# Kernel tuning notes

Measured on AMD Instinct MI355X. Metric: run time of the kernel, lower is better.

## Reference

```python
import jax, jax.numpy as jnp
import numpy as np

E = 32          # embed_size; each node embedding is an [E, E] matrix
V = 50257       # vocab size
L = 2048        # number of leaves (complete binary tree)
N = 2 * L - 1   # total nodes, post-order-compatible layout (children before parent)
LBL = 128       # label_size


def setup_inputs() -> dict:
    key = jax.random.key(0)
    k1, k2, k3 = jax.random.split(key, 3)
    words = jax.random.randint(k1, (N,), 0, V, dtype=jnp.int32)
    # complete binary tree: nodes 0..L-1 are leaves; internal node i has
    # children 2*(i-L) and 2*(i-L)+1, which always have smaller indices.
    left = np.zeros(N, dtype=np.int32)
    right = np.zeros(N, dtype=np.int32)
    ii = np.arange(L, N)
    left[L:] = 2 * (ii - L)
    right[L:] = left[L:] + 1
    is_leaf = np.arange(N) < L
    # xavier-ish init scale for embedding ([V, E*E]) and projection
    emb = jax.random.normal(k2, (V, E * E), dtype=jnp.float32) * (1.0 / E)
    bias = jnp.zeros((E, E), dtype=jnp.float32)
    W_proj = jax.random.normal(k3, (LBL, E * E), dtype=jnp.float32) * 0.02
    b_proj = jnp.zeros((LBL,), dtype=jnp.float32)
    return {
        "words": words,
        "left": jnp.asarray(left),
        "right": jnp.asarray(right),
        "is_leaf": jnp.asarray(is_leaf),
        "emb": emb,
        "bias": bias,
        "W_proj": W_proj,
        "b_proj": b_proj,
        "label": 3,
    }


def reference(words, left, right, is_leaf, emb, bias, W_proj, b_proj, label):
    n = words.shape[0]
    e = bias.shape[0]
    states0 = jnp.zeros((n, e, e), dtype=emb.dtype)

    def step(states, x):
        i, w, li, ri, leaf = x
        Wn = emb[w].reshape(e, e)                    # node embedding matrix
        l = states[li]                               # [E, E] child state
        r = states[ri]
        comp = l @ (Wn @ r) + bias                   # RNTN composition
        val = jnp.where(leaf, jax.nn.relu(Wn), jax.nn.relu(comp))
        return states.at[i].set(val), None

    xs = (jnp.arange(n), words, left, right, is_leaf)
    states, _ = jax.lax.scan(step, states0, xs)

    root = states[-1].reshape(-1)                    # [E*E]
    logits = root @ W_proj.T + b_proj                # [LBL]
    loss = -jax.nn.log_softmax(logits)[label]        # CrossEntropyLoss, batch=1
    prediction = jnp.argmax(logits)
    return prediction, loss
```

## Files before the change

### kernel.cpp

```cpp
#include <hip/hip_runtime.h>
#include <math.h>


#define EE 1024
typedef float4 f4;

__device__ __forceinline__ f4 relu4(f4 v) {
    v.x = fmaxf(v.x, 0.f); v.y = fmaxf(v.y, 0.f);
    v.z = fmaxf(v.z, 0.f); v.w = fmaxf(v.w, 0.f);
    return v;
}
__device__ __forceinline__ f4 fma4s(float s, f4 b, f4 a) {
    a.x = fmaf(s, b.x, a.x); a.y = fmaf(s, b.y, a.y);
    a.z = fmaf(s, b.z, a.z); a.w = fmaf(s, b.w, a.w);
    return a;
}
__device__ __forceinline__ f4 addrelu4(f4 a, f4 b) {
    a.x = fmaxf(a.x + b.x, 0.f); a.y = fmaxf(a.y + b.y, 0.f);
    a.z = fmaxf(a.z + b.z, 0.f); a.w = fmaxf(a.w + b.w, 0.f);
    return a;
}
__device__ __forceinline__ void lds_fence() {
    asm volatile("s_waitcnt lgkmcnt(0)" ::: "memory");
    __builtin_amdgcn_sched_barrier(0);
}
__device__ __forceinline__ void load_row(f4 d[4], const float* __restrict__ src, int lane) {
    #pragma unroll
    for (int i = 0; i < 4; ++i) d[i] = ((const f4*)src)[lane + 64 * i];
}

__device__ __forceinline__ void node_wave(
    const f4 wv[4], bool reluKids,
    const float* __restrict__ Lsrc, const float* __restrict__ Rsrc,
    const float* __restrict__ bias, int lane,
    float* sA, float* sB, float* gdst)
{
    f4 rv[4], lv[4];
    load_row(rv, Rsrc, lane);
    load_row(lv, Lsrc, lane);
    if (reluKids) {
        #pragma unroll
        for (int i = 0; i < 4; ++i) { rv[i] = relu4(rv[i]); lv[i] = relu4(lv[i]); }
    }
    #pragma unroll
    for (int i = 0; i < 4; ++i) {
        ((f4*)sA)[lane + 64 * i] = wv[i];
        ((f4*)sB)[lane + 64 * i] = rv[i];
    }
    lds_fence();

    const int tr = lane >> 3, tc = lane & 7;
    const f4 z = {0.f, 0.f, 0.f, 0.f};
    f4 t0 = z, t1 = z, t2 = z, t3 = z;
    #pragma unroll
    for (int k = 0; k < 32; k += 4) {
        f4 a0 = *(const f4*)(sA + (4 * tr + 0) * 32 + k);
        f4 a1 = *(const f4*)(sA + (4 * tr + 1) * 32 + k);
        f4 a2 = *(const f4*)(sA + (4 * tr + 2) * 32 + k);
        f4 a3 = *(const f4*)(sA + (4 * tr + 3) * 32 + k);
        f4 b0 = *(const f4*)(sB + (k + 0) * 32 + 4 * tc);
        f4 b1 = *(const f4*)(sB + (k + 1) * 32 + 4 * tc);
        f4 b2 = *(const f4*)(sB + (k + 2) * 32 + 4 * tc);
        f4 b3 = *(const f4*)(sB + (k + 3) * 32 + 4 * tc);
        t0 = fma4s(a0.x, b0, fma4s(a0.y, b1, fma4s(a0.z, b2, fma4s(a0.w, b3, t0))));
        t1 = fma4s(a1.x, b0, fma4s(a1.y, b1, fma4s(a1.z, b2, fma4s(a1.w, b3, t1))));
        t2 = fma4s(a2.x, b0, fma4s(a2.y, b1, fma4s(a2.z, b2, fma4s(a2.w, b3, t2))));
        t3 = fma4s(a3.x, b0, fma4s(a3.y, b1, fma4s(a3.z, b2, fma4s(a3.w, b3, t3))));
    }
    __builtin_amdgcn_sched_barrier(0);
    *(f4*)(sA + (4 * tr + 0) * 32 + 4 * tc) = t0;
    *(f4*)(sA + (4 * tr + 1) * 32 + 4 * tc) = t1;
    *(f4*)(sA + (4 * tr + 2) * 32 + 4 * tc) = t2;
    *(f4*)(sA + (4 * tr + 3) * 32 + 4 * tc) = t3;
    #pragma unroll
    for (int i = 0; i < 4; ++i) ((f4*)sB)[lane + 64 * i] = lv[i];
    lds_fence();

    f4 s0 = z, s1 = z, s2 = z, s3 = z;
    #pragma unroll
    for (int k = 0; k < 32; k += 4) {
        f4 a0 = *(const f4*)(sB + (4 * tr + 0) * 32 + k);
        f4 a1 = *(const f4*)(sB + (4 * tr + 1) * 32 + k);
        f4 a2 = *(const f4*)(sB + (4 * tr + 2) * 32 + k);
        f4 a3 = *(const f4*)(sB + (4 * tr + 3) * 32 + k);
        f4 b0 = *(const f4*)(sA + (k + 0) * 32 + 4 * tc);
        f4 b1 = *(const f4*)(sA + (k + 1) * 32 + 4 * tc);
        f4 b2 = *(const f4*)(sA + (k + 2) * 32 + 4 * tc);
        f4 b3 = *(const f4*)(sA + (k + 3) * 32 + 4 * tc);
        s0 = fma4s(a0.x, b0, fma4s(a0.y, b1, fma4s(a0.z, b2, fma4s(a0.w, b3, s0))));
        s1 = fma4s(a1.x, b0, fma4s(a1.y, b1, fma4s(a1.z, b2, fma4s(a1.w, b3, s1))));
        s2 = fma4s(a2.x, b0, fma4s(a2.y, b1, fma4s(a2.z, b2, fma4s(a2.w, b3, s2))));
        s3 = fma4s(a3.x, b0, fma4s(a3.y, b1, fma4s(a3.z, b2, fma4s(a3.w, b3, s3))));
    }
    s0 = addrelu4(s0, *(const f4*)(bias + (4 * tr + 0) * 32 + 4 * tc));
    s1 = addrelu4(s1, *(const f4*)(bias + (4 * tr + 1) * 32 + 4 * tc));
    s2 = addrelu4(s2, *(const f4*)(bias + (4 * tr + 2) * 32 + 4 * tc));
    s3 = addrelu4(s3, *(const f4*)(bias + (4 * tr + 3) * 32 + 4 * tc));
    *(f4*)(sB + (4 * tr + 0) * 32 + 4 * tc) = s0;
    *(f4*)(sB + (4 * tr + 1) * 32 + 4 * tc) = s1;
    *(f4*)(sB + (4 * tr + 2) * 32 + 4 * tc) = s2;
    *(f4*)(sB + (4 * tr + 3) * 32 + 4 * tc) = s3;
    if (gdst) {
        *(f4*)(gdst + (4 * tr + 0) * 32 + 4 * tc) = s0;
        *(f4*)(gdst + (4 * tr + 1) * 32 + 4 * tc) = s1;
        *(f4*)(gdst + (4 * tr + 2) * 32 + 4 * tc) = s2;
        *(f4*)(gdst + (4 * tr + 3) * 32 + 4 * tc) = s3;
    }
}

template<bool LEAF>
__global__ __launch_bounds__(256) void subtree_kernel(
    const int* __restrict__ words, const float* __restrict__ emb,
    const float* __restrict__ bias, float* __restrict__ states,
    int rootBase, int nCompute, const float* __restrict__ warm, int warmN, int L)
{
    __shared__ float sBuf[8 * EE];
    const int bid = blockIdx.x;
    const int t = threadIdx.x, w = t >> 6, lane = t & 63;
    if (bid >= nCompute) {
        float acc = 0.f;
        for (int i = (bid - nCompute) * 256 + t; i < 128 * EE / 4; i += warmN * 256) {
            const f4 v = ((const f4*)warm)[i];
            acc += v.x + v.y + v.z + v.w;
        }
        asm volatile("" :: "v"(acc));
        return;
    }
    const int root = rootBase + bid;
    const int c1i = 2 * (root - L) + (w >> 1);
    const int nbi = 2 * (c1i - L) + (w & 1);
    f4 wv[4], wx[4], wr[4];
    load_row(wv, emb + (size_t)words[nbi] * EE, lane);
    if (w < 2) load_row(wx, emb + (size_t)words[2 * (root - L) + w] * EE, lane);
    if (w == 0) load_row(wr, emb + (size_t)words[root] * EE, lane);
    const int li = 2 * (nbi - L), ri = li + 1;
    const float *Lp, *Rp;
    if (LEAF) { Lp = emb + (size_t)words[li] * EE;        Rp = emb + (size_t)words[ri] * EE; }
    else      { Lp = states + (size_t)(li - L) * EE;      Rp = states + (size_t)(ri - L) * EE; }

    node_wave(wv, LEAF, Lp, Rp, bias, lane,
              sBuf + 2 * w * EE, sBuf + (2 * w + 1) * EE, nullptr);
    __syncthreads();
    if (w < 2)
        node_wave(wx, false, sBuf + (4 * w + 1) * EE, sBuf + (4 * w + 3) * EE,
                  bias, lane, sBuf + 4 * w * EE, sBuf + (4 * w + 2) * EE, nullptr);
    __syncthreads();
    if (w == 0)
        node_wave(wr, false, sBuf + 2 * EE, sBuf + 6 * EE, bias, lane,
                  sBuf + 0 * EE, sBuf + 4 * EE, states + (size_t)(root - L) * EE);
}

__global__ __launch_bounds__(1024) void tail_kernel(
    const int* __restrict__ words, const float* __restrict__ emb,
    const float* __restrict__ bias, float* __restrict__ states,
    const float* __restrict__ W_proj, const float* __restrict__ b_proj,
    const int* __restrict__ label, float* __restrict__ out, int L, int N)
{
    __shared__ float sBuf[6 * EE];
    __shared__ float sLog[128];
    const int t = threadIdx.x, w = t >> 6, lane = t & 63;
    const int rootN = N - 1;

    f4 wv[4], wr[4];
    if (w < 2) {
        const int n = rootN - 2 + w;
        load_row(wv, emb + (size_t)words[n] * EE, lane);
        if (w == 0) load_row(wr, emb + (size_t)words[rootN] * EE, lane);
        const int li = 2 * (n - L), ri = li + 1;
        node_wave(wv, false, states + (size_t)(li - L) * EE,
                  states + (size_t)(ri - L) * EE, bias, lane,
                  sBuf + 2 * w * EE, sBuf + (2 * w + 1) * EE, nullptr);
    } else {
        float acc = 0.f;
        for (int i = t - 128; i < 128 * EE / 4; i += 896) {
            const f4 v = ((const f4*)W_proj)[i];
            acc += v.x + v.y + v.z + v.w;
        }
        asm volatile("" :: "v"(acc));
    }
    __syncthreads();
    if (w == 0)
        node_wave(wr, false, sBuf + 1 * EE, sBuf + 3 * EE, bias, lane,
                  sBuf + 4 * EE, sBuf + 5 * EE, nullptr);
    __syncthreads();

    const float* root = sBuf + 5 * EE;
    {
        const int j = t >> 3, part = t & 7;
        const float* Wr = W_proj + (size_t)j * EE + part * 128;
        const float* rt = root + part * 128;
        float acc = 0.f;
        #pragma unroll
        for (int k = 0; k < 128; k += 4) {
            const f4 w4 = *(const f4*)(Wr + k);
            const f4 r4 = *(const f4*)(rt + k);
            acc = fmaf(w4.x, r4.x, acc);
            acc = fmaf(w4.y, r4.y, acc);
            acc = fmaf(w4.z, r4.z, acc);
            acc = fmaf(w4.w, r4.w, acc);
        }
        acc += __shfl_xor(acc, 1);
        acc += __shfl_xor(acc, 2);
        acc += __shfl_xor(acc, 4);
        if (part == 0) sLog[j] = acc + b_proj[j];
    }
    __syncthreads();

    if (t < 64) {
        const float v0 = sLog[t], v1 = sLog[t + 64];
        float m; int mi;
        if (v1 > v0) { m = v1; mi = t + 64; } else { m = v0; mi = t; }
        #pragma unroll
        for (int d = 1; d < 64; d <<= 1) {
            const float om = __shfl_xor(m, d);
            const int omi = __shfl_xor(mi, d);
            if (om > m || (om == m && omi < mi)) { m = om; mi = omi; }
        }
        float se = expf(v0 - m) + expf(v1 - m);
        #pragma unroll
        for (int d = 1; d < 64; d <<= 1) se += __shfl_xor(se, d);
        if (t == 0) {
            out[0] = (float)mi;
            out[1] = -(sLog[label[0]] - m - logf(se));
        }
    }
}

extern "C" void kernel_launch(void* const* d_in, const int* in_sizes, int n_in,
                              void* d_out, int out_size, void* d_ws, size_t ws_size,
                              hipStream_t stream) {
    (void)n_in; (void)out_size; (void)ws_size;
    const int*   words  = (const int*)  d_in[0];
    const float* emb    = (const float*)d_in[4];
    const float* bias   = (const float*)d_in[5];
    const float* W_proj = (const float*)d_in[6];
    const float* b_proj = (const float*)d_in[7];
    const int*   label  = (const int*)  d_in[8];
    float* out    = (float*)d_out;
    float* states = (float*)d_ws;

    const int N = in_sizes[0];
    const int L = (N + 1) / 2;

    const int lv3 = L + L / 2 + L / 4;
    const int lv6 = lv3 + L / 8 + L / 16 + L / 32;
    const int lv9 = lv6 + L / 64 + L / 128 + L / 256;

    subtree_kernel<true><<<256, 256, 0, stream>>>(
        words, emb, bias, states, lv3, 256, W_proj, 8, L);
    subtree_kernel<false><<<40, 256, 0, stream>>>(
        words, emb, bias, states, lv6, 32, W_proj, 8, L);
    subtree_kernel<false><<<12, 256, 0, stream>>>(
        words, emb, bias, states, lv9, 4, W_proj, 8, L);
    tail_kernel<<<1, 1024, 0, stream>>>(
        words, emb, bias, states, W_proj, b_proj, label, out, L, N);
}
```

Before: 65.81 us.

## Fuse tree-level kernels into one cooperative kernel with grid syncs

Replaces the four sequential launches (three subtree levels plus the tail) with a single cooperative kernel of L/8 blocks that separates levels with grid-wide syncs. Block 0 then performs the top levels, projection and softmax itself. This removes the per-launch overhead and the gaps between kernels, in exchange for grid barrier costs and the requirement that all 256 blocks be co-resident. If the cooperative launch fails, the code falls back to the old multi-kernel path.

```diff
diff --git a/kernel.cpp b/kernel.cpp
--- a/kernel.cpp
+++ b/kernel.cpp
@@ -1,5 +1,8 @@
 #include <hip/hip_runtime.h>
+#include <hip/hip_cooperative_groups.h>
 #include <math.h>
+
+namespace cg = cooperative_groups;
 
 
 #define EE 1024
@@ -109,24 +112,11 @@
 }
 
 template<bool LEAF>
-__global__ __launch_bounds__(256) void subtree_kernel(
+__device__ __forceinline__ void do_subtree(
     const int* __restrict__ words, const float* __restrict__ emb,
     const float* __restrict__ bias, float* __restrict__ states,
-    int rootBase, int nCompute, const float* __restrict__ warm, int warmN, int L)
-{
-    __shared__ float sBuf[8 * EE];
-    const int bid = blockIdx.x;
-    const int t = threadIdx.x, w = t >> 6, lane = t & 63;
-    if (bid >= nCompute) {
-        float acc = 0.f;
-        for (int i = (bid - nCompute) * 256 + t; i < 128 * EE / 4; i += warmN * 256) {
-            const f4 v = ((const f4*)warm)[i];
-            acc += v.x + v.y + v.z + v.w;
-        }
-        asm volatile("" :: "v"(acc));
-        return;
-    }
-    const int root = rootBase + bid;
+    int root, int L, int w, int lane, float* sBuf)
+{
     const int c1i = 2 * (root - L) + (w >> 1);
     const int nbi = 2 * (c1i - L) + (w & 1);
     f4 wv[4], wx[4], wr[4];
@@ -135,8 +125,8 @@
     if (w == 0) load_row(wr, emb + (size_t)words[root] * EE, lane);
     const int li = 2 * (nbi - L), ri = li + 1;
     const float *Lp, *Rp;
-    if (LEAF) { Lp = emb + (size_t)words[li] * EE;        Rp = emb + (size_t)words[ri] * EE; }
-    else      { Lp = states + (size_t)(li - L) * EE;      Rp = states + (size_t)(ri - L) * EE; }
+    if (LEAF) { Lp = emb + (size_t)words[li] * EE;   Rp = emb + (size_t)words[ri] * EE; }
+    else      { Lp = states + (size_t)(li - L) * EE; Rp = states + (size_t)(ri - L) * EE; }
 
     node_wave(wv, LEAF, Lp, Rp, bias, lane,
               sBuf + 2 * w * EE, sBuf + (2 * w + 1) * EE, nullptr);
@@ -148,6 +138,129 @@
     if (w == 0)
         node_wave(wr, false, sBuf + 2 * EE, sBuf + 6 * EE, bias, lane,
                   sBuf + 0 * EE, sBuf + 4 * EE, states + (size_t)(root - L) * EE);
+}
+
+__global__ __launch_bounds__(256) void rntn_coop(
+    const int* __restrict__ words, const float* __restrict__ emb,
+    const float* __restrict__ bias, float* __restrict__ states,
+    const float* __restrict__ W_proj, const float* __restrict__ b_proj,
+    const int* __restrict__ label, float* __restrict__ out, int L, int N)
+{
+    __shared__ float sBuf[8 * EE];
+    __shared__ float sLog[128];
+    const int t = threadIdx.x, w = t >> 6, lane = t & 63;
+    const int bid = blockIdx.x;
+    const int lv3 = L + L / 2 + L / 4;
+    const int lv6 = lv3 + L / 8 + L / 16 + L / 32;
+    const int lv9 = lv6 + L / 64 + L / 128 + L / 256;
+
+    do_subtree<true>(words, emb, bias, states, lv3 + bid, L, w, lane, sBuf);
+    cg::this_grid().sync();
+
+    if (bid < L / 64) {
+        do_subtree<false>(words, emb, bias, states, lv6 + bid, L, w, lane, sBuf);
+    } else if (bid < L / 64 + 32) {
+        float acc = 0.f;
+        for (int i = (bid - L / 64) * 256 + t; i < 128 * EE / 4; i += 32 * 256) {
+            const f4 v = ((const f4*)W_proj)[i];
+            acc += v.x + v.y + v.z + v.w;
+        }
+        asm volatile("" :: "v"(acc));
+    }
+    cg::this_grid().sync();
+
+    if (bid < L / 512) {
+        do_subtree<false>(words, emb, bias, states, lv9 + bid, L, w, lane, sBuf);
+    } else if (bid >= 8 && (bid & 7) == 0) {
+        const int slot = (bid >> 3) - 1;
+        float acc = 0.f;
+        for (int i = slot * 256 + t; i < 128 * EE / 4; i += 31 * 256) {
+            const f4 v = ((const f4*)W_proj)[i];
+            acc += v.x + v.y + v.z + v.w;
+        }
+        asm volatile("" :: "v"(acc));
+    }
+    cg::this_grid().sync();
+    if (bid != 0) return;
+
+    {
+        const int rootN = N - 1;
+        f4 wv[4], wr[4];
+        if (w < 2) {
+            const int n = rootN - 2 + w;
+            load_row(wv, emb + (size_t)words[n] * EE, lane);
+            if (w == 0) load_row(wr, emb + (size_t)words[rootN] * EE, lane);
+            const int li = 2 * (n - L);
+            node_wave(wv, false, states + (size_t)(li - L) * EE,
+                      states + (size_t)(li + 1 - L) * EE, bias, lane,
+                      sBuf + 2 * w * EE, sBuf + (2 * w + 1) * EE, nullptr);
+        }
+        __syncthreads();
+        if (w == 0)
+            node_wave(wr, false, sBuf + 1 * EE, sBuf + 3 * EE, bias, lane,
+                      sBuf + 4 * EE, sBuf + 5 * EE, nullptr);
+        __syncthreads();
+    }
+
+    const float* root = sBuf + 5 * EE;
+    {
+        const int j = t >> 1, part = t & 1;
+        const float* Wr = W_proj + (size_t)j * EE + part * 512;
+        const float* rt = root + part * 512;
+        float acc = 0.f;
+        #pragma unroll 4
+        for (int k = 0; k < 512; k += 4) {
+            const f4 w4 = *(const f4*)(Wr + k);
+            const f4 r4 = *(const f4*)(rt + k);
+            acc = fmaf(w4.x, r4.x, acc);
+            acc = fmaf(w4.y, r4.y, acc);
+            acc = fmaf(w4.z, r4.z, acc);
+            acc = fmaf(w4.w, r4.w, acc);
+        }
+        acc += __shfl_xor(acc, 1);
+        if (part == 0) sLog[j] = acc + b_proj[j];
+    }
+    __syncthreads();
+
+    if (t < 64) {
+        const float v0 = sLog[t], v1 = sLog[t + 64];
+        float m; int mi;
+        if (v1 > v0) { m = v1; mi = t + 64; } else { m = v0; mi = t; }
+        #pragma unroll
+        for (int d = 1; d < 64; d <<= 1) {
+            const float om = __shfl_xor(m, d);
+            const int omi = __shfl_xor(mi, d);
+            if (om > m || (om == m && omi < mi)) { m = om; mi = omi; }
+        }
+        float se = expf(v0 - m) + expf(v1 - m);
+        #pragma unroll
+        for (int d = 1; d < 64; d <<= 1) se += __shfl_xor(se, d);
+        if (t == 0) {
+            out[0] = (float)mi;
+            out[1] = -(sLog[label[0]] - m - logf(se));
+        }
+    }
+}
+
+template<bool LEAF>
+__global__ __launch_bounds__(256) void subtree_kernel(
+    const int* __restrict__ words, const float* __restrict__ emb,
+    const float* __restrict__ bias, float* __restrict__ states,
+    int rootBase, int nCompute, const float* __restrict__ warm, int warmN, int L)
+{
+    __shared__ float sBuf[8 * EE];
+    const int bid = blockIdx.x;
+    const int t = threadIdx.x, w = t >> 6, lane = t & 63;
+    if (bid >= nCompute) {
+        float acc = 0.f;
+        for (int i = (bid - nCompute) * 256 + t; i < 128 * EE / 4; i += warmN * 256) {
+            const f4 v = ((const f4*)warm)[i];
+            acc += v.x + v.y + v.z + v.w;
+        }
+        asm volatile("" :: "v"(acc));
+        return;
+    }
+    do_subtree<LEAF>(words, emb, bias, states, rootBase + bid, L, w, lane, sBuf);
 }
 
 __global__ __launch_bounds__(1024) void tail_kernel(
@@ -239,19 +352,28 @@
     float* out    = (float*)d_out;
     float* states = (float*)d_ws;
 
-    const int N = in_sizes[0];
-    const int L = (N + 1) / 2;
-
-    const int lv3 = L + L / 2 + L / 4;
-    const int lv6 = lv3 + L / 8 + L / 16 + L / 32;
-    const int lv9 = lv6 + L / 64 + L / 128 + L / 256;
-
-    subtree_kernel<true><<<256, 256, 0, stream>>>(
-        words, emb, bias, states, lv3, 256, W_proj, 8, L);
-    subtree_kernel<false><<<40, 256, 0, stream>>>(
-        words, emb, bias, states, lv6, 32, W_proj, 8, L);
-    subtree_kernel<false><<<12, 256, 0, stream>>>(
-        words, emb, bias, states, lv9, 4, W_proj, 8, L);
-    tail_kernel<<<1, 1024, 0, stream>>>(
-        words, emb, bias, states, W_proj, b_proj, label, out, L, N);
-}
+    int N = in_sizes[0];
+    int L = (N + 1) / 2;
+
+    void* kargs[] = {
+        (void*)&words, (void*)&emb, (void*)&bias, (void*)&states,
+        (void*)&W_proj, (void*)&b_proj, (void*)&label, (void*)&out,
+        (void*)&L, (void*)&N
+    };
+    hipError_t err = hipLaunchCooperativeKernel(
+        (const void*)rntn_coop, dim3(L / 8), dim3(256), kargs, 0, stream);
+    if (err != hipSuccess) {
+        (void)hipGetLastError();
+        const int lv3 = L + L / 2 + L / 4;
+        const int lv6 = lv3 + L / 8 + L / 16 + L / 32;
+        const int lv9 = lv6 + L / 64 + L / 128 + L / 256;
+        subtree_kernel<true><<<256, 256, 0, stream>>>(
+            words, emb, bias, states, lv3, 256, W_proj, 8, L);
+        subtree_kernel<false><<<40, 256, 0, stream>>>(
+            words, emb, bias, states, lv6, 32, W_proj, 8, L);
+        subtree_kernel<false><<<12, 256, 0, stream>>>(
+            words, emb, bias, states, lv9, 4, W_proj, 8, L);
+        tail_kernel<<<1, 1024, 0, stream>>>(
+            words, emb, bias, states, W_proj, b_proj, label, out, L, N);
+    }
+}
```

After: 150.9 us (median of 2 runs). +129.3%, slower.

## Fuse all tree levels into one kernel with last-block tail via atomic counter

Applied to the files above, without the earlier changes.

Replaces the four launches (three subtree levels plus the tail) with a single kernel. Each 1024-thread block reduces a 32-leaf subtree entirely in LDS, and the last block to arrive, detected with an atomic counter, computes the top levels and the projection. It also prefetches the next level's embedding row while the current node runs and warms W_proj with idle waves. The goal is to remove inter-kernel launch gaps and global round trips. The cost is a serial tail in one block, a memset launch, and a 128KB LDS footprint per block.

```diff
diff --git a/kernel.cpp b/kernel.cpp
--- a/kernel.cpp
+++ b/kernel.cpp
@@ -20,20 +20,24 @@
     a.z = fmaxf(a.z + b.z, 0.f); a.w = fmaxf(a.w + b.w, 0.f);
     return a;
 }
-__device__ __forceinline__ void lds_fence() {
+__device__ __forceinline__ void fence_all() {
+    asm volatile("s_waitcnt vmcnt(0) lgkmcnt(0)" ::: "memory");
+    __builtin_amdgcn_sched_barrier(0);
+}
+__device__ __forceinline__ void fence_lds() {
     asm volatile("s_waitcnt lgkmcnt(0)" ::: "memory");
     __builtin_amdgcn_sched_barrier(0);
 }
-__device__ __forceinline__ void load_row(f4 d[4], const float* __restrict__ src, int lane) {
+__device__ __forceinline__ void load_row(f4 d[4], const float* src, int lane) {
     #pragma unroll
     for (int i = 0; i < 4; ++i) d[i] = ((const f4*)src)[lane + 64 * i];
 }
 
 __device__ __forceinline__ void node_wave(
-    const f4 wv[4], bool reluKids,
-    const float* __restrict__ Lsrc, const float* __restrict__ Rsrc,
+    f4 wv[4], bool reluKids,
+    const float* Lsrc, const float* Rsrc,
     const float* __restrict__ bias, int lane,
-    float* sA, float* sB, float* gdst)
+    float* sA, float* sB, float* gdst, const float* nextW)
 {
     f4 rv[4], lv[4];
     load_row(rv, Rsrc, lane);
@@ -42,12 +46,14 @@
         #pragma unroll
         for (int i = 0; i < 4; ++i) { rv[i] = relu4(rv[i]); lv[i] = relu4(lv[i]); }
     }
+    fence_all();
     #pragma unroll
     for (int i = 0; i < 4; ++i) {
         ((f4*)sA)[lane + 64 * i] = wv[i];
         ((f4*)sB)[lane + 64 * i] = rv[i];
     }
-    lds_fence();
+    if (nextW) load_row(wv, nextW, lane);
+    fence_lds();
 
     const int tr = lane >> 3, tc = lane & 7;
     const f4 z = {0.f, 0.f, 0.f, 0.f};
@@ -74,7 +80,7 @@
     *(f4*)(sA + (4 * tr + 3) * 32 + 4 * tc) = t3;
     #pragma unroll
     for (int i = 0; i < 4; ++i) ((f4*)sB)[lane + 64 * i] = lv[i];
-    lds_fence();
+    fence_lds();
 
     f4 s0 = z, s1 = z, s2 = z, s3 = z;
     #pragma unroll
@@ -108,83 +114,113 @@
     }
 }
 
-template<bool LEAF>
-__global__ __launch_bounds__(256) void subtree_kernel(
-    const int* __restrict__ words, const float* __restrict__ emb,
-    const float* __restrict__ bias, float* __restrict__ states,
-    int rootBase, int nCompute, const float* __restrict__ warm, int warmN, int L)
-{
-    __shared__ float sBuf[8 * EE];
-    const int bid = blockIdx.x;
-    const int t = threadIdx.x, w = t >> 6, lane = t & 63;
-    if (bid >= nCompute) {
-        float acc = 0.f;
-        for (int i = (bid - nCompute) * 256 + t; i < 128 * EE / 4; i += warmN * 256) {
-            const f4 v = ((const f4*)warm)[i];
-            acc += v.x + v.y + v.z + v.w;
-        }
-        asm volatile("" :: "v"(acc));
-        return;
-    }
-    const int root = rootBase + bid;
-    const int c1i = 2 * (root - L) + (w >> 1);
-    const int nbi = 2 * (c1i - L) + (w & 1);
-    f4 wv[4], wx[4], wr[4];
-    load_row(wv, emb + (size_t)words[nbi] * EE, lane);
-    if (w < 2) load_row(wx, emb + (size_t)words[2 * (root - L) + w] * EE, lane);
-    if (w == 0) load_row(wr, emb + (size_t)words[root] * EE, lane);
-    const int li = 2 * (nbi - L), ri = li + 1;
-    const float *Lp, *Rp;
-    if (LEAF) { Lp = emb + (size_t)words[li] * EE;        Rp = emb + (size_t)words[ri] * EE; }
-    else      { Lp = states + (size_t)(li - L) * EE;      Rp = states + (size_t)(ri - L) * EE; }
-
-    node_wave(wv, LEAF, Lp, Rp, bias, lane,
-              sBuf + 2 * w * EE, sBuf + (2 * w + 1) * EE, nullptr);
-    __syncthreads();
-    if (w < 2)
-        node_wave(wx, false, sBuf + (4 * w + 1) * EE, sBuf + (4 * w + 3) * EE,
-                  bias, lane, sBuf + 4 * w * EE, sBuf + (4 * w + 2) * EE, nullptr);
-    __syncthreads();
-    if (w == 0)
-        node_wave(wr, false, sBuf + 2 * EE, sBuf + 6 * EE, bias, lane,
-                  sBuf + 0 * EE, sBuf + 4 * EE, states + (size_t)(root - L) * EE);
-}
-
-__global__ __launch_bounds__(1024) void tail_kernel(
+__global__ __launch_bounds__(1024, 4) void rntn_all(
     const int* __restrict__ words, const float* __restrict__ emb,
     const float* __restrict__ bias, float* __restrict__ states,
     const float* __restrict__ W_proj, const float* __restrict__ b_proj,
-    const int* __restrict__ label, float* __restrict__ out, int L, int N)
+    const int* __restrict__ label, float* __restrict__ out,
+    unsigned int* __restrict__ cnt, int L)
 {
-    __shared__ float sBuf[6 * EE];
-    __shared__ float sLog[128];
+    __shared__ float sBuf[32 * EE];
+    __shared__ int sLast;
     const int t = threadIdx.x, w = t >> 6, lane = t & 63;
-    const int rootN = N - 1;
-
-    f4 wv[4], wr[4];
-    if (w < 2) {
-        const int n = rootN - 2 + w;
+    const int b = blockIdx.x;
+    const int twoL = 2 * L;
+
+    {
+        const int n1 = L + (b << 4) + w;
+        f4 wv[4];
+        load_row(wv, emb + (size_t)words[n1] * EE, lane);
+        const int li = 2 * (n1 - L);
+        const int n2 = twoL - (twoL >> 2) + (b << 3) + w;
+        node_wave(wv, true,
+                  emb + (size_t)words[li] * EE, emb + (size_t)words[li + 1] * EE,
+                  bias, lane, sBuf + (2 * w) * EE, sBuf + (2 * w + 1) * EE,
+                  nullptr, (w < 8) ? emb + (size_t)words[n2] * EE : nullptr);
+        __syncthreads();
+        for (int r = 2; r <= 5; ++r) {
+            const int c = 1 << (5 - r);
+            if (w < c) {
+                const int st = 1 << r;
+                const int node = twoL - (twoL >> r) + (b << (5 - r)) + w;
+                const int nn = twoL - (twoL >> (r + 1)) + (b << (4 - r)) + w;
+                node_wave(wv, false,
+                          sBuf + (st * w + (st >> 2)) * EE,
+                          sBuf + (st * w + 3 * (st >> 2)) * EE,
+                          bias, lane,
+                          sBuf + (st * w) * EE, sBuf + (st * w + (st >> 1)) * EE,
+                          (r == 5) ? states + (size_t)(node - L) * EE : nullptr,
+                          (r < 5 && w < (c >> 1)) ? emb + (size_t)words[nn] * EE
+                                                  : nullptr);
+            } else if (r == 2 && w >= 8) {
+                const f4 v = ((const f4*)W_proj)[(b * 8 + (w - 8)) * 64 + lane];
+                float a = v.x + v.y + v.z + v.w;
+                asm volatile("" :: "v"(a));
+            }
+            __syncthreads();
+        }
+    }
+
+    if (t == 0) {
+        __threadfence();
+        const unsigned old = atomicAdd(cnt, 1u);
+        sLast = (old == (unsigned)(gridDim.x - 1)) ? 1 : 0;
+    }
+    __syncthreads();
+    if (!sLast) return;
+    __threadfence();
+
+    f4 wv[4];
+    {
+        const int lvb6 = twoL - (twoL >> 6);
+        int n = lvb6 + w;
         load_row(wv, emb + (size_t)words[n] * EE, lane);
-        if (w == 0) load_row(wr, emb + (size_t)words[rootN] * EE, lane);
-        const int li = 2 * (n - L), ri = li + 1;
-        node_wave(wv, false, states + (size_t)(li - L) * EE,
-                  states + (size_t)(ri - L) * EE, bias, lane,
-                  sBuf + 2 * w * EE, sBuf + (2 * w + 1) * EE, nullptr);
-    } else {
-        float acc = 0.f;
-        for (int i = t - 128; i < 128 * EE / 4; i += 896) {
-            const f4 v = ((const f4*)W_proj)[i];
-            acc += v.x + v.y + v.z + v.w;
-        }
-        asm volatile("" :: "v"(acc));
-    }
-    __syncthreads();
-    if (w == 0)
-        node_wave(wr, false, sBuf + 1 * EE, sBuf + 3 * EE, bias, lane,
-                  sBuf + 4 * EE, sBuf + 5 * EE, nullptr);
-    __syncthreads();
-
-    const float* root = sBuf + 5 * EE;
+        const float* c0 = states + (size_t)(2 * (n - L) - L) * EE;
+        node_wave(wv, false, c0, c0 + EE, bias, lane,
+                  sBuf + (2 * w) * EE, sBuf + (2 * w + 1) * EE,
+                  states + (size_t)(n - L) * EE,
+                  emb + (size_t)words[n + 16] * EE);
+        n = lvb6 + 16 + w;
+        c0 = states + (size_t)(2 * (n - L) - L) * EE;
+        const int n7 = twoL - (twoL >> 7) + w;
+        node_wave(wv, false, c0, c0 + EE, bias, lane,
+                  sBuf + (2 * w) * EE, sBuf + (2 * w + 1) * EE,
+                  states + (size_t)(n - L) * EE,
+                  emb + (size_t)words[n7] * EE);
+        __syncthreads();
+        c0 = states + (size_t)(2 * (n7 - L) - L) * EE;
+        node_wave(wv, false, c0, c0 + EE, bias, lane,
+                  sBuf + (16 + w) * EE, sBuf + w * EE, nullptr,
+                  (w < 8) ? emb + (size_t)words[twoL - (twoL >> 8) + w] * EE
+                          : nullptr);
+        __syncthreads();
+    }
+    for (int r = 8; r <= 11; ++r) {
+        const int c = 1 << (11 - r);
+        if (w < c) {
+            const int st = 1 << (r - 7);
+            const int nn = twoL - (twoL >> (r + 1)) + w;
+            node_wave(wv, false,
+                      sBuf + (st * w) * EE, sBuf + (st * w + (st >> 1)) * EE,
+                      bias, lane,
+                      sBuf + (16 + w) * EE, sBuf + (st * w) * EE, nullptr,
+                      (r < 11 && w < (c >> 1)) ? emb + (size_t)words[nn] * EE
+                                               : nullptr);
+        } else {
+            const int nIdle = 16 - c, k = w - c;
+            const int base = (r - 8) * 8192;
+            float a = 0.f;
+            for (int i = k * 64 + lane; i < 8192; i += nIdle * 64) {
+                const f4 v = ((const f4*)W_proj)[base + i];
+                a += v.x + v.y + v.z + v.w;
+            }
+            asm volatile("" :: "v"(a));
+        }
+        __syncthreads();
+    }
+
+    const float* root = sBuf;
+    float* sLog = sBuf + EE;
     {
         const int j = t >> 3, part = t & 7;
         const float* Wr = W_proj + (size_t)j * EE + part * 128;
@@ -242,16 +278,9 @@
     const int N = in_sizes[0];
     const int L = (N + 1) / 2;
 
-    const int lv3 = L + L / 2 + L / 4;
-    const int lv6 = lv3 + L / 8 + L / 16 + L / 32;
-    const int lv9 = lv6 + L / 64 + L / 128 + L / 256;
-
-    subtree_kernel<true><<<256, 256, 0, stream>>>(
-        words, emb, bias, states, lv3, 256, W_proj, 8, L);
-    subtree_kernel<false><<<40, 256, 0, stream>>>(
-        words, emb, bias, states, lv6, 32, W_proj, 8, L);
-    subtree_kernel<false><<<12, 256, 0, stream>>>(
-        words, emb, bias, states, lv9, 4, W_proj, 8, L);
-    tail_kernel<<<1, 1024, 0, stream>>>(
-        words, emb, bias, states, W_proj, b_proj, label, out, L, N);
-}
+    unsigned int* cnt = (unsigned int*)(states + (size_t)(N - 1 - L) * EE);
+    hipMemsetAsync(cnt, 0, sizeof(unsigned int), stream);
+
+    rntn_all<<<L / 32, 1024, 0, stream>>>(
+        words, emb, bias, states, W_proj, b_proj, label, out, cnt, L);
+}
```

Measured after the change: 147.4 us. 124% more time.

## Fuse subtree levels and tail into one kernel via last-block atomic counters

Applied to the files above, without the earlier changes.

Replaces the four dependent launches (three subtree levels plus the tail) with a single kernel. Blocks advance up the tree with a last-arriver pattern: per-group atomic counters with thread fences decide which block continues to the next level, and the final block does the root and the projection. This removes inter-kernel launch gaps and tail drain, at the cost of an added memset of the counters and more serialised work inside the last surviving blocks. The projection is also repartitioned from 8 to 2 threads per label.

```diff
diff --git a/kernel.cpp b/kernel.cpp
--- a/kernel.cpp
+++ b/kernel.cpp
@@ -24,7 +24,7 @@
     asm volatile("s_waitcnt lgkmcnt(0)" ::: "memory");
     __builtin_amdgcn_sched_barrier(0);
 }
-__device__ __forceinline__ void load_row(f4 d[4], const float* __restrict__ src, int lane) {
+__device__ __forceinline__ void load_row(f4 d[4], const float* src, int lane) {
     #pragma unroll
     for (int i = 0; i < 4; ++i) d[i] = ((const f4*)src)[lane + 64 * i];
 }
@@ -109,24 +109,11 @@
 }
 
 template<bool LEAF>
-__global__ __launch_bounds__(256) void subtree_kernel(
+__device__ __forceinline__ void do_subtree(
     const int* __restrict__ words, const float* __restrict__ emb,
     const float* __restrict__ bias, float* __restrict__ states,
-    int rootBase, int nCompute, const float* __restrict__ warm, int warmN, int L)
+    int root, int L, int w, int lane, float* sBuf)
 {
-    __shared__ float sBuf[8 * EE];
-    const int bid = blockIdx.x;
-    const int t = threadIdx.x, w = t >> 6, lane = t & 63;
-    if (bid >= nCompute) {
-        float acc = 0.f;
-        for (int i = (bid - nCompute) * 256 + t; i < 128 * EE / 4; i += warmN * 256) {
-            const f4 v = ((const f4*)warm)[i];
-            acc += v.x + v.y + v.z + v.w;
-        }
-        asm volatile("" :: "v"(acc));
-        return;
-    }
-    const int root = rootBase + bid;
     const int c1i = 2 * (root - L) + (w >> 1);
     const int nbi = 2 * (c1i - L) + (w & 1);
     f4 wv[4], wx[4], wr[4];
@@ -135,8 +122,8 @@
     if (w == 0) load_row(wr, emb + (size_t)words[root] * EE, lane);
     const int li = 2 * (nbi - L), ri = li + 1;
     const float *Lp, *Rp;
-    if (LEAF) { Lp = emb + (size_t)words[li] * EE;        Rp = emb + (size_t)words[ri] * EE; }
-    else      { Lp = states + (size_t)(li - L) * EE;      Rp = states + (size_t)(ri - L) * EE; }
+    if (LEAF) { Lp = emb + (size_t)words[li] * EE;   Rp = emb + (size_t)words[ri] * EE; }
+    else      { Lp = states + (size_t)(li - L) * EE; Rp = states + (size_t)(ri - L) * EE; }
 
     node_wave(wv, LEAF, Lp, Rp, bias, lane,
               sBuf + 2 * w * EE, sBuf + (2 * w + 1) * EE, nullptr);
@@ -150,48 +137,90 @@
                   sBuf + 0 * EE, sBuf + 4 * EE, states + (size_t)(root - L) * EE);
 }
 
-__global__ __launch_bounds__(1024) void tail_kernel(
+__global__ __launch_bounds__(256) void rntn_chain(
     const int* __restrict__ words, const float* __restrict__ emb,
     const float* __restrict__ bias, float* __restrict__ states,
     const float* __restrict__ W_proj, const float* __restrict__ b_proj,
-    const int* __restrict__ label, float* __restrict__ out, int L, int N)
+    const int* __restrict__ label, float* __restrict__ out,
+    unsigned int* __restrict__ cnt, int L)
 {
-    __shared__ float sBuf[6 * EE];
+    __shared__ float sBuf[8 * EE];
     __shared__ float sLog[128];
+    __shared__ int sFlag;
     const int t = threadIdx.x, w = t >> 6, lane = t & 63;
-    const int rootN = N - 1;
-
-    f4 wv[4], wr[4];
-    if (w < 2) {
-        const int n = rootN - 2 + w;
-        load_row(wv, emb + (size_t)words[n] * EE, lane);
-        if (w == 0) load_row(wr, emb + (size_t)words[rootN] * EE, lane);
-        const int li = 2 * (n - L), ri = li + 1;
-        node_wave(wv, false, states + (size_t)(li - L) * EE,
-                  states + (size_t)(ri - L) * EE, bias, lane,
-                  sBuf + 2 * w * EE, sBuf + (2 * w + 1) * EE, nullptr);
-    } else {
-        float acc = 0.f;
-        for (int i = t - 128; i < 128 * EE / 4; i += 896) {
+    const int b = blockIdx.x;
+    const int twoL = 2 * L;
+    const int lv3 = twoL - (twoL >> 3);
+    const int lv6 = twoL - (twoL >> 6);
+    const int lv9 = twoL - (twoL >> 9);
+
+    do_subtree<true>(words, emb, bias, states, lv3 + b, L, w, lane, sBuf);
+    {
+        const int i = b * 256 + t;
+        if (i < 128 * EE / 4) {
             const f4 v = ((const f4*)W_proj)[i];
-            acc += v.x + v.y + v.z + v.w;
-        }
-        asm volatile("" :: "v"(acc));
-    }
-    __syncthreads();
-    if (w == 0)
-        node_wave(wr, false, sBuf + 1 * EE, sBuf + 3 * EE, bias, lane,
-                  sBuf + 4 * EE, sBuf + 5 * EE, nullptr);
-    __syncthreads();
+            float a = v.x + v.y + v.z + v.w;
+            asm volatile("" :: "v"(a));
+        }
+    }
+    __syncthreads();
+    if (t == 0) {
+        __threadfence();
+        sFlag = (atomicAdd(&cnt[b >> 3], 1u) == 7u) ? 1 : 0;
+    }
+    __syncthreads();
+    if (!sFlag) return;
+    __threadfence();
+
+    const int gB = b >> 3;
+    do_subtree<false>(words, emb, bias, states, lv6 + gB, L, w, lane, sBuf);
+    __syncthreads();
+    if (t == 0) {
+        __threadfence();
+        sFlag = (atomicAdd(&cnt[32 + (gB >> 3)], 1u) == 7u) ? 1 : 0;
+    }
+    __syncthreads();
+    if (!sFlag) return;
+    __threadfence();
+
+    const int gC = gB >> 3;
+    do_subtree<false>(words, emb, bias, states, lv9 + gC, L, w, lane, sBuf);
+    __syncthreads();
+    if (t == 0) {
+        __threadfence();
+        sFlag = (atomicAdd(&cnt[36], 1u) == 3u) ? 1 : 0;
+    }
+    __syncthreads();
+    if (!sFlag) return;
+    __threadfence();
+
+    {
+        const int rootN = twoL - 2;
+        f4 wv[4], wr[4];
+        if (w < 2) {
+            const int n = rootN - 2 + w;
+            load_row(wv, emb + (size_t)words[n] * EE, lane);
+            if (w == 0) load_row(wr, emb + (size_t)words[rootN] * EE, lane);
+            const int li = 2 * (n - L);
+            node_wave(wv, false, states + (size_t)(li - L) * EE,
+                      states + (size_t)(li + 1 - L) * EE, bias, lane,
+                      sBuf + 2 * w * EE, sBuf + (2 * w + 1) * EE, nullptr);
+        }
+        __syncthreads();
+        if (w == 0)
+            node_wave(wr, false, sBuf + 1 * EE, sBuf + 3 * EE, bias, lane,
+                      sBuf + 4 * EE, sBuf + 5 * EE, nullptr);
+        __syncthreads();
+    }
 
     const float* root = sBuf + 5 * EE;
     {
-        const int j = t >> 3, part = t & 7;
-        const float* Wr = W_proj + (size_t)j * EE + part * 128;
-        const float* rt = root + part * 128;
+        const int j = t >> 1, part = t & 1;
+        const float* Wr = W_proj + (size_t)j * EE + part * 512;
+        const float* rt = root + part * 512;
         float acc = 0.f;
-        #pragma unroll
-        for (int k = 0; k < 128; k += 4) {
+        #pragma unroll 4
+        for (int k = 0; k < 512; k += 4) {
             const f4 w4 = *(const f4*)(Wr + k);
             const f4 r4 = *(const f4*)(rt + k);
             acc = fmaf(w4.x, r4.x, acc);
@@ -200,8 +229,6 @@
             acc = fmaf(w4.w, r4.w, acc);
         }
         acc += __shfl_xor(acc, 1);
-        acc += __shfl_xor(acc, 2);
-        acc += __shfl_xor(acc, 4);
         if (part == 0) sLog[j] = acc + b_proj[j];
     }
     __syncthreads();
@@ -242,16 +269,9 @@
     const int N = in_sizes[0];
     const int L = (N + 1) / 2;
 
-    const int lv3 = L + L / 2 + L / 4;
-    const int lv6 = lv3 + L / 8 + L / 16 + L / 32;
-    const int lv9 = lv6 + L / 64 + L / 128 + L / 256;
-
-    subtree_kernel<true><<<256, 256, 0, stream>>>(
-        words, emb, bias, states, lv3, 256, W_proj, 8, L);
-    subtree_kernel<false><<<40, 256, 0, stream>>>(
-        words, emb, bias, states, lv6, 32, W_proj, 8, L);
-    subtree_kernel<false><<<12, 256, 0, stream>>>(
-        words, emb, bias, states, lv9, 4, W_proj, 8, L);
-    tail_kernel<<<1, 1024, 0, stream>>>(
-        words, emb, bias, states, W_proj, b_proj, label, out, L, N);
-}
+    unsigned int* cnt = (unsigned int*)states;
+    hipMemsetAsync(cnt, 0, 64 * sizeof(unsigned int), stream);
+
+    rntn_chain<<<L / 8, 256, 0, stream>>>(
+        words, emb, bias, states, W_proj, b_proj, label, out, cnt, L);
+}
```

After: 89.57 us. 1.36x slower.
